# Optimization experiments

Measured on AMD Instinct MI355X. Metric: run time of the kernel, lower is better.

The kernel has to match this reference:

```python
import jax, jax.numpy as jnp
import numpy as np

B, N, Q, M, OUT = 8192, 512, 6, 1024, 256
QUANTILE_COEFFS = np.array([-3.0, -0.834, -0.248, 0.248, 0.834], dtype=np.float32)


def setup_inputs() -> dict:
    key = jax.random.key(0)
    k1, k2, k3, k4, k5, k6, k7 = jax.random.split(key, 7)
    x = jax.random.normal(k1, (B, N), dtype=jnp.float32)
    beta = jnp.zeros((N,), dtype=jnp.float32)
    gamma = jnp.ones((N,), dtype=jnp.float32)
    w = jax.random.normal(k2, (N * Q + M, OUT), dtype=jnp.float32)
    biases = jax.random.normal(k3, (1,), dtype=jnp.float32)
    # chosen_index rows: (count, n1, q1, n2, q2); n-indices in [0,N), q-indices in [0,Q)
    cnt = jnp.arange(M, dtype=jnp.int64)[:, None]
    n1 = jax.random.randint(k4, (M, 1), 0, N)
    q1 = jax.random.randint(k5, (M, 1), 0, Q)
    n2 = jax.random.randint(k6, (M, 1), 0, N)
    q2 = jax.random.randint(k7, (M, 1), 0, Q)
    chosen_index = jnp.concatenate([cnt, n1, q1, n2, q2], axis=1).astype(jnp.int64)
    return {"x": x, "beta": beta, "gamma": gamma, "w": w, "biases": biases,
            "chosen_index": chosen_index}


def reference(x, beta, gamma, w, biases, chosen_index):
    # Batch norm (EMA with decay=0.5 after register+update collapses to batch stats)
    mean = jnp.mean(x, axis=0)                      # (N,)
    var = jnp.var(x, axis=0)                        # (N,) biased, like unbiased=False
    normed = gamma * (x - mean) / jnp.sqrt(var + 0.001) + beta   # (B, N)
    # Maxout: base ReLU + 5 quantile-thresholded branches
    coeffs = jnp.asarray(QUANTILE_COEFFS)           # (5,)
    quant = coeffs[:, None] * var[None, :] + mean[None, :]       # (5, N)
    base = jnp.maximum(0.0, normed)[None]                        # (1, B, N)
    branches = jnp.maximum(0.0, normed[None] - quant[:, None, :] * gamma + beta)  # (5, B, N)
    stacked = jnp.concatenate([base, branches], axis=0)          # (Q, B, N)
    max_x = jnp.transpose(stacked, (1, 2, 0))                    # (B, N, Q)
    # Minout (test mode): per-row gather of two (n,q) coords, elementwise min
    n1, q1 = chosen_index[:, 1], chosen_index[:, 2]
    n2, q2 = chosen_index[:, 3], chosen_index[:, 4]
    D1 = max_x[:, n1, q1]                                        # (B, M)
    D2 = max_x[:, n2, q2]                                        # (B, M)
    min_x = jnp.minimum(D1, D2)                                  # (B, M)
    feat = jnp.concatenate([max_x.reshape(x.shape[0], -1), min_x], axis=1)  # (B, N*Q+M)
    output = feat @ w + biases                                   # (B, OUT)
    return output
```

## Files before the change

kernel.cpp:

```cpp
#include <hip/hip_runtime.h>
#include <stdint.h>

typedef unsigned int uint32;
typedef unsigned short u16;
typedef __attribute__((ext_vector_type(8))) short bf16x8;
typedef __attribute__((ext_vector_type(4))) float f32x4;

#define WS_SCALE 0
#define WS_SHIFT 512
#define WS_SUBQ  1024
#define WS_SHSUB 4096
#define WS_PSUM  8192
#define WS_PSQ   (8192+131072)
#define WRT_OFF  (2u<<20)
#define AMIN_OFF (4u<<20)
#define PART_OFF (21u<<20)

__device__ __forceinline__ u16 f2bf(float f){
  uint32 u; __builtin_memcpy(&u,&f,4);
  u = u + 0x7fffu + ((u>>16)&1u);
  return (u16)(u>>16);
}
__device__ __forceinline__ float bf2f(u16 b){
  uint32 u = ((uint32)b)<<16; float f; __builtin_memcpy(&f,&u,4); return f;
}
__device__ __forceinline__ uint32 pk2(float a, float b){
  return (uint32)f2bf(a) | ((uint32)f2bf(b)<<16);
}
__device__ __forceinline__ void gll16(u16* lds, const u16* g){
  __builtin_amdgcn_global_load_lds((const __attribute__((address_space(1))) uint32*)g,
                                   (__attribute__((address_space(3))) uint32*)lds, 16, 0, 0);
}

__global__ __launch_bounds__(512) void k_pre(const float* __restrict__ x,
                                             const float* __restrict__ w,
                                             float* __restrict__ ws,
                                             u16* __restrict__ wrT){
  int b = blockIdx.x, t = threadIdx.x;
  if (b < 256){
    const float* xp = x + (size_t)b*32*512 + t;
    float sum = 0.f, sq = 0.f;
    #pragma unroll 8
    for (int r=0; r<32; ++r){ float v = xp[(size_t)r*512]; sum += v; sq += v*v; }
    ws[WS_PSUM + b*512 + t] = sum;
    ws[WS_PSQ  + b*512 + t] = sq;
  } else {
    int c2 = b - 256;
    int o = t & 255, half = t >> 8;
    int swzrow = (o >> 1) & 3;
    u16* dst = wrT + (size_t)c2*8192 + o*32;
    #pragma unroll
    for (int gi=0; gi<2; ++gi){
      int g = half*2 + gi;
      union { bf16x8 v; u16 h[8]; } R;
      #pragma unroll
      for (int e=0; e<8; ++e){
        int k = g*8 + e;
        int sk;
        if (c2 < 96) sk = ((c2 & 15)*32 + k)*6 + (c2 >> 4);
        else         sk = 3072 + (c2 - 96)*32 + k;
        R.h[e] = f2bf(w[(size_t)sk*256 + o]);
      }
      *(bf16x8*)(dst + ((g ^ swzrow)*8)) = R.v;
    }
  }
}

__global__ __launch_bounds__(512) void k_stats_final(const float* __restrict__ beta,
                                                     const float* __restrict__ gamma,
                                                     float* __restrict__ ws){
  __shared__ float rs[16][32], rq[16][32];
  int t = threadIdx.x;
  int nl = t & 31, sl = t >> 5;
  int n = blockIdx.x*32 + nl;
  float sum=0.f, sq=0.f;
  #pragma unroll
  for (int j=0;j<16;++j){
    int p = sl*16 + j;
    sum += ws[WS_PSUM + p*512 + n];
    sq  += ws[WS_PSQ  + p*512 + n];
  }
  rs[sl][nl]=sum; rq[sl][nl]=sq;
  __syncthreads();
  if (sl==0){
    #pragma unroll
    for (int j=1;j<16;++j){ sum+=rs[j][nl]; sq+=rq[j][nl]; }
    float mean = sum * (1.0f/8192.0f);
    float var  = sq  * (1.0f/8192.0f) - mean*mean;
    float g = gamma[n], b = beta[n];
    float inv = 1.0f / sqrtf(var + 0.001f);
    float scale = g * inv;
    float shift = b - mean*scale;
    ws[WS_SCALE + n] = scale;
    ws[WS_SHIFT + n] = shift;
    const float QC[5] = {-3.0f, -0.834f, -0.248f, 0.248f, 0.834f};
    ws[WS_SUBQ  + n] = 0.f;
    ws[WS_SHSUB + n] = shift;
    #pragma unroll
    for (int c=0; c<5; ++c){
      float sub = (QC[c]*var + mean)*g - b;
      ws[WS_SUBQ  + (c+1)*512 + n] = sub;
      ws[WS_SHSUB + (c+1)*512 + n] = shift - sub;
    }
  }
}

__global__ __launch_bounds__(256) void k_minfeat(const float* __restrict__ x,
                                                 const float* __restrict__ ws,
                                                 const int* __restrict__ ci,
                                                 u16* __restrict__ amin){
  __shared__ float nrm[8][512];
  __shared__ uint32 tnn[1024];
  __shared__ float ts1[1024];
  __shared__ float ts2[1024];
  int t = threadIdx.x;
  int b0 = blockIdx.x * 8;
  #pragma unroll
  for (int ii=0; ii<4; ++ii){
    int i = ii*256 + t;
    int n1 = ci[i*5+1], q1 = ci[i*5+2], n2 = ci[i*5+3], q2 = ci[i*5+4];
    tnn[i] = (uint32)n1 | ((uint32)n2 << 16);
    ts1[i] = ws[WS_SUBQ + q1*512 + n1];
    ts2[i] = ws[WS_SUBQ + q2*512 + n2];
  }
  {
    int r = t >> 5, c0 = (t & 31) * 16;
    const float* xr = x + (size_t)(b0 + r)*512 + c0;
    #pragma unroll
    for (int j=0;j<4;++j){
      float4 v  = *(const float4*)(xr + j*4);
      float4 sc = *(const float4*)(ws + WS_SCALE + c0 + j*4);
      float4 sh = *(const float4*)(ws + WS_SHIFT + c0 + j*4);
      float4 o; o.x=fmaf(v.x,sc.x,sh.x); o.y=fmaf(v.y,sc.y,sh.y);
      o.z=fmaf(v.z,sc.z,sh.z); o.w=fmaf(v.w,sc.w,sh.w);
      *(float4*)(&nrm[r][c0+j*4]) = o;
    }
  }
  __syncthreads();
  int m0 = t*4;
  uint4  nn = *(const uint4*)(&tnn[m0]);
  float4 s1 = *(const float4*)(&ts1[m0]);
  float4 s2 = *(const float4*)(&ts2[m0]);
  int cc = m0 >> 5, k = m0 & 31, g2 = k >> 3;
  #pragma unroll
  for (int r=0;r<8;++r){
    float v0 = fminf(fmaxf(nrm[r][nn.x & 0xffff] - s1.x, 0.f), fmaxf(nrm[r][nn.x >> 16] - s2.x, 0.f));
    float v1 = fminf(fmaxf(nrm[r][nn.y & 0xffff] - s1.y, 0.f), fmaxf(nrm[r][nn.y >> 16] - s2.y, 0.f));
    float v2 = fminf(fmaxf(nrm[r][nn.z & 0xffff] - s1.z, 0.f), fmaxf(nrm[r][nn.z >> 16] - s2.z, 0.f));
    float v3 = fminf(fmaxf(nrm[r][nn.w & 0xffff] - s1.w, 0.f), fmaxf(nrm[r][nn.w >> 16] - s2.w, 0.f));
    int pos = cc*32 + ((g2 ^ (((b0 + r) >> 1) & 3))*8) + (k & 7);
    uint2 pv; pv.x = pk2(v0,v1); pv.y = pk2(v2,v3);
    *(uint2*)(amin + (size_t)(b0 + r)*1024 + pos) = pv;
  }
}

__global__ __launch_bounds__(512,4) void k_gemm(const float* __restrict__ x,
                                                const float* __restrict__ ws,
                                                const u16* __restrict__ wrT,
                                                const u16* __restrict__ amin,
                                                u16* __restrict__ parts){
  __shared__ u16 wt[2][8192];
  __shared__ u16 ft[2][4096];
  __shared__ float pscale[512];
  __shared__ float pshsub[512];

  int t = threadIdx.x;
  int d = blockIdx.x;
  int mtile = d & 63, s = d >> 6;
  int brow = mtile * 128;
  bool isMin = (s >= 6);

  if (!isMin){
    pscale[t] = ws[WS_SCALE + t];
    pshsub[t] = ws[WS_SHSUB + s*512 + t];
  }

  int row = t >> 2, g = t & 3;
  int ftw = row*32 + ((g ^ ((row >> 1) & 3))*8);
  int wuni = t & ~63;
  const float* xrow = x + (size_t)(brow + row)*512;
  const u16* aminrow = amin + (size_t)(brow + row)*1024 + (isMin ? (s-6)*512 : 0) + g*8;
  const u16* wbase = wrT + (size_t)(s*16)*8192;

  int lane = t & 63, wv = t >> 6;
  int wm = wv >> 2, wn = wv & 3;
  int lr = lane & 15, lk = lane >> 4;
  int g16 = (lk ^ ((lr >> 1) & 3)) * 8;
  f32x4 acc[4][4] = {};
  float4 xa[2][2];

  auto loadX = [&](int cc, int xb){
    int col = cc*32 + g*8;
    xa[xb][0] = *(const float4*)(xrow + col);
    xa[xb][1] = *(const float4*)(xrow + col + 4);
  };
  auto stageW = [&](int cc, int nb){
    const u16* wsrc = wbase + (size_t)cc*8192;
    gll16(&wt[nb][wuni*8], wsrc + (size_t)t*8);
    gll16(&wt[nb][4096 + wuni*8], wsrc + 4096 + (size_t)t*8);
    if (isMin) gll16(&ft[nb][wuni*8], aminrow + cc*32);
  };
  auto packFT = [&](int cc, int nb, int xb){
    int col = cc*32 + g*8;
    float4 a0 = xa[xb][0], a1 = xa[xb][1];
    float4 sc0 = *(const float4*)(pscale + col);
    float4 sc1 = *(const float4*)(pscale + col + 4);
    float4 h0  = *(const float4*)(pshsub + col);
    float4 h1  = *(const float4*)(pshsub + col + 4);
    union { bf16x8 v; uint32 u[4]; } R;
    R.u[0] = pk2(fmaxf(fmaf(a0.x,sc0.x,h0.x),0.f), fmaxf(fmaf(a0.y,sc0.y,h0.y),0.f));
    R.u[1] = pk2(fmaxf(fmaf(a0.z,sc0.z,h0.z),0.f), fmaxf(fmaf(a0.w,sc0.w,h0.w),0.f));
    R.u[2] = pk2(fmaxf(fmaf(a1.x,sc1.x,h1.x),0.f), fmaxf(fmaf(a1.y,sc1.y,h1.y),0.f));
    R.u[3] = pk2(fmaxf(fmaf(a1.z,sc1.z,h1.z),0.f), fmaxf(fmaf(a1.w,sc1.w,h1.w),0.f));
    *(bf16x8*)(&ft[nb][ftw]) = R.v;
  };
  auto compute = [&](int cb){
    bf16x8 A[4], Bv[4];
    #pragma unroll
    for (int mi=0; mi<4; ++mi)
      A[mi] = *(const bf16x8*)(&ft[cb][(wm*64 + mi*16 + lr)*32 + g16]);
    #pragma unroll
    for (int ni=0; ni<4; ++ni)
      Bv[ni] = *(const bf16x8*)(&wt[cb][(wn*64 + ni*16 + lr)*32 + g16]);
    #pragma unroll
    for (int mi=0; mi<4; ++mi)
      #pragma unroll
      for (int ni=0; ni<4; ++ni)
        acc[mi][ni] = __builtin_amdgcn_mfma_f32_16x16x32_bf16(A[mi], Bv[ni], acc[mi][ni], 0, 0, 0);
  };

  __syncthreads();
  if (!isMin) loadX(0, 0);
  stageW(0, 0);
  if (!isMin){ packFT(0, 0, 0); loadX(1, 1); }
  __syncthreads();

  int cur = 0;
  for (int c=0; c<16; ++c){
    if (!isMin && c < 14) loadX(c+2, c & 1);
    if (c < 15){
      stageW(c+1, cur^1);
      if (!isMin) packFT(c+1, cur^1, (c+1) & 1);
    }
    compute(cur);
    __syncthreads();
    cur ^= 1;
  }

  u16* pp = parts + ((size_t)s*8192 + brow)*256;
  #pragma unroll
  for (int mi=0; mi<4; ++mi)
    #pragma unroll
    for (int ni=0; ni<4; ++ni)
      #pragma unroll
      for (int r=0; r<4; ++r){
        int rl = wm*64 + mi*16 + lk*4 + r;
        int cl = wn*64 + ni*16 + lr;
        pp[(size_t)rl*256 + cl] = f2bf(acc[mi][ni][r]);
      }
}

__global__ __launch_bounds__(256) void k_reduce(const u16* __restrict__ parts,
                                                const float* __restrict__ biases,
                                                float* __restrict__ out){
  int i = (blockIdx.x*256 + threadIdx.x) * 8;
  float b = biases[0];
  float a[8];
  #pragma unroll
  for (int j=0;j<8;++j) a[j] = b;
  #pragma unroll
  for (int s2=0;s2<8;++s2){
    bf16x8 v = *(const bf16x8*)(parts + (size_t)s2*2097152 + i);
    #pragma unroll
    for (int j=0;j<8;++j) a[j] += bf2f((u16)v[j]);
  }
  float4 o0 = {a[0],a[1],a[2],a[3]}, o1 = {a[4],a[5],a[6],a[7]};
  *(float4*)(out + i) = o0;
  *(float4*)(out + i + 4) = o1;
}

extern "C" void kernel_launch(void* const* d_in, const int* in_sizes, int n_in,
                              void* d_out, int out_size, void* d_ws, size_t ws_size,
                              hipStream_t stream){
  const float* x      = (const float*)d_in[0];
  const float* beta   = (const float*)d_in[1];
  const float* gamma  = (const float*)d_in[2];
  const float* w      = (const float*)d_in[3];
  const float* biases = (const float*)d_in[4];
  const int*   ci     = (const int*)d_in[5];
  float* out = (float*)d_out;
  float* wsf = (float*)d_ws;
  u16* wrT   = (u16*)((char*)d_ws + WRT_OFF);
  u16* amin  = (u16*)((char*)d_ws + AMIN_OFF);
  u16* parts = (u16*)((char*)d_ws + PART_OFF);

  k_pre         <<<384, 512, 0, stream>>>(x, w, wsf, wrT);
  k_stats_final <<<16,  512, 0, stream>>>(beta, gamma, wsf);
  k_minfeat     <<<1024,256, 0, stream>>>(x, wsf, ci, amin);
  k_gemm        <<<512, 512, 0, stream>>>(x, wsf, wrT, amin, parts);
  k_reduce      <<<1024,256, 0, stream>>>(parts, biases, out);
}
```

Measured before the change: 54.55 us.

## Fuse split-K reduction into GEMM via last-block atomic counter

```diff
diff --git a/kernel.cpp b/kernel.cpp
--- a/kernel.cpp
+++ b/kernel.cpp
@@ -12,6 +12,7 @@
 #define WS_SHSUB 4096
 #define WS_PSUM  8192
 #define WS_PSQ   (8192+131072)
+#define CNT_OFF  0x180000u
 #define WRT_OFF  (2u<<20)
 #define AMIN_OFF (4u<<20)
 #define PART_OFF (21u<<20)
@@ -158,11 +159,15 @@
                                                 const float* __restrict__ ws,
                                                 const u16* __restrict__ wrT,
                                                 const u16* __restrict__ amin,
-                                                u16* __restrict__ parts){
+                                                const float* __restrict__ biases,
+                                                u16* __restrict__ parts,
+                                                int* __restrict__ cnt,
+                                                float* __restrict__ out){
   __shared__ u16 wt[2][8192];
   __shared__ u16 ft[2][4096];
   __shared__ float pscale[512];
   __shared__ float pshsub[512];
+  __shared__ int lastFlag;
 
   int t = threadIdx.x;
   int d = blockIdx.x;
@@ -258,25 +263,37 @@
         int cl = wn*64 + ni*16 + lr;
         pp[(size_t)rl*256 + cl] = f2bf(acc[mi][ni][r]);
       }
-}
-
-__global__ __launch_bounds__(256) void k_reduce(const u16* __restrict__ parts,
-                                                const float* __restrict__ biases,
-                                                float* __restrict__ out){
-  int i = (blockIdx.x*256 + threadIdx.x) * 8;
-  float b = biases[0];
-  float a[8];
-  #pragma unroll
-  for (int j=0;j<8;++j) a[j] = b;
-  #pragma unroll
-  for (int s2=0;s2<8;++s2){
-    bf16x8 v = *(const bf16x8*)(parts + (size_t)s2*2097152 + i);
-    #pragma unroll
-    for (int j=0;j<8;++j) a[j] += bf2f((u16)v[j]);
-  }
-  float4 o0 = {a[0],a[1],a[2],a[3]}, o1 = {a[4],a[5],a[6],a[7]};
-  *(float4*)(out + i) = o0;
-  *(float4*)(out + i + 4) = o1;
+
+  __threadfence();
+  __syncthreads();
+  if (t == 0){
+    int old = atomicAdd(cnt + mtile, 1);
+    lastFlag = (old == 7);
+  }
+  __syncthreads();
+  if (lastFlag){
+    __threadfence();
+    float b0 = biases[0];
+    const u16* pb = parts + (size_t)brow*256;
+    float* op = out + (size_t)brow*256;
+    #pragma unroll
+    for (int it=0; it<8; ++it){
+      int task = it*512 + t;
+      int rowi = task >> 5, cg = task & 31;
+      float a[8];
+      #pragma unroll
+      for (int j=0;j<8;++j) a[j] = b0;
+      #pragma unroll
+      for (int s2=0;s2<8;++s2){
+        bf16x8 v = *(const bf16x8*)(pb + (size_t)s2*2097152 + rowi*256 + cg*8);
+        #pragma unroll
+        for (int j=0;j<8;++j) a[j] += bf2f((u16)v[j]);
+      }
+      float4 o0 = {a[0],a[1],a[2],a[3]}, o1 = {a[4],a[5],a[6],a[7]};
+      *(float4*)(op + rowi*256 + cg*8) = o0;
+      *(float4*)(op + rowi*256 + cg*8 + 4) = o1;
+    }
+  }
 }
 
 extern "C" void kernel_launch(void* const* d_in, const int* in_sizes, int n_in,
@@ -293,10 +310,11 @@
   u16* wrT   = (u16*)((char*)d_ws + WRT_OFF);
   u16* amin  = (u16*)((char*)d_ws + AMIN_OFF);
   u16* parts = (u16*)((char*)d_ws + PART_OFF);
-
+  int* cnt   = (int*)((char*)d_ws + CNT_OFF);
+
+  hipMemsetAsync(cnt, 0, 64*sizeof(int), stream);
   k_pre         <<<384, 512, 0, stream>>>(x, w, wsf, wrT);
   k_stats_final <<<16,  512, 0, stream>>>(beta, gamma, wsf);
   k_minfeat     <<<1024,256, 0, stream>>>(x, wsf, ci, amin);
-  k_gemm        <<<512, 512, 0, stream>>>(x, wsf, wrT, amin, parts);
-  k_reduce      <<<1024,256, 0, stream>>>(parts, biases, out);
-}
+  k_gemm        <<<512, 512, 0, stream>>>(x, wsf, wrT, amin, biases, parts, cnt, out);
+}
```

New measurement: 214.3 us. 3.93x slower.

## Fuse min-feature computation into GEMM blocks that consume it

Applied to the files above, without the earlier changes.

```diff
diff --git a/kernel.cpp b/kernel.cpp
--- a/kernel.cpp
+++ b/kernel.cpp
@@ -105,59 +105,11 @@
   }
 }
 
-__global__ __launch_bounds__(256) void k_minfeat(const float* __restrict__ x,
-                                                 const float* __restrict__ ws,
-                                                 const int* __restrict__ ci,
-                                                 u16* __restrict__ amin){
-  __shared__ float nrm[8][512];
-  __shared__ uint32 tnn[1024];
-  __shared__ float ts1[1024];
-  __shared__ float ts2[1024];
-  int t = threadIdx.x;
-  int b0 = blockIdx.x * 8;
-  #pragma unroll
-  for (int ii=0; ii<4; ++ii){
-    int i = ii*256 + t;
-    int n1 = ci[i*5+1], q1 = ci[i*5+2], n2 = ci[i*5+3], q2 = ci[i*5+4];
-    tnn[i] = (uint32)n1 | ((uint32)n2 << 16);
-    ts1[i] = ws[WS_SUBQ + q1*512 + n1];
-    ts2[i] = ws[WS_SUBQ + q2*512 + n2];
-  }
-  {
-    int r = t >> 5, c0 = (t & 31) * 16;
-    const float* xr = x + (size_t)(b0 + r)*512 + c0;
-    #pragma unroll
-    for (int j=0;j<4;++j){
-      float4 v  = *(const float4*)(xr + j*4);
-      float4 sc = *(const float4*)(ws + WS_SCALE + c0 + j*4);
-      float4 sh = *(const float4*)(ws + WS_SHIFT + c0 + j*4);
-      float4 o; o.x=fmaf(v.x,sc.x,sh.x); o.y=fmaf(v.y,sc.y,sh.y);
-      o.z=fmaf(v.z,sc.z,sh.z); o.w=fmaf(v.w,sc.w,sh.w);
-      *(float4*)(&nrm[r][c0+j*4]) = o;
-    }
-  }
-  __syncthreads();
-  int m0 = t*4;
-  uint4  nn = *(const uint4*)(&tnn[m0]);
-  float4 s1 = *(const float4*)(&ts1[m0]);
-  float4 s2 = *(const float4*)(&ts2[m0]);
-  int cc = m0 >> 5, k = m0 & 31, g2 = k >> 3;
-  #pragma unroll
-  for (int r=0;r<8;++r){
-    float v0 = fminf(fmaxf(nrm[r][nn.x & 0xffff] - s1.x, 0.f), fmaxf(nrm[r][nn.x >> 16] - s2.x, 0.f));
-    float v1 = fminf(fmaxf(nrm[r][nn.y & 0xffff] - s1.y, 0.f), fmaxf(nrm[r][nn.y >> 16] - s2.y, 0.f));
-    float v2 = fminf(fmaxf(nrm[r][nn.z & 0xffff] - s1.z, 0.f), fmaxf(nrm[r][nn.z >> 16] - s2.z, 0.f));
-    float v3 = fminf(fmaxf(nrm[r][nn.w & 0xffff] - s1.w, 0.f), fmaxf(nrm[r][nn.w >> 16] - s2.w, 0.f));
-    int pos = cc*32 + ((g2 ^ (((b0 + r) >> 1) & 3))*8) + (k & 7);
-    uint2 pv; pv.x = pk2(v0,v1); pv.y = pk2(v2,v3);
-    *(uint2*)(amin + (size_t)(b0 + r)*1024 + pos) = pv;
-  }
-}
-
 __global__ __launch_bounds__(512,4) void k_gemm(const float* __restrict__ x,
                                                 const float* __restrict__ ws,
                                                 const u16* __restrict__ wrT,
-                                                const u16* __restrict__ amin,
+                                                const int* __restrict__ ci,
+                                                u16* __restrict__ amin,
                                                 u16* __restrict__ parts){
   __shared__ u16 wt[2][8192];
   __shared__ u16 ft[2][4096];
@@ -173,6 +125,59 @@
   if (!isMin){
     pscale[t] = ws[WS_SCALE + t];
     pshsub[t] = ws[WS_SHSUB + s*512 + t];
+  } else {
+    int h = s - 6;
+    float*  nrmL = (float*)&wt[0][0];
+    uint32* tnnL = (uint32*)&ft[0][0];
+    float*  ts1L = (float*)&ft[0][0] + 512;
+    float*  ts2L = (float*)&ft[0][0] + 1024;
+    {
+      int gm = h*512 + t;
+      int n1 = ci[gm*5+1], q1 = ci[gm*5+2], n2 = ci[gm*5+3], q2 = ci[gm*5+4];
+      tnnL[t] = (uint32)n1 | ((uint32)n2 << 16);
+      ts1L[t] = ws[WS_SUBQ + q1*512 + n1];
+      ts2L[t] = ws[WS_SUBQ + q2*512 + n2];
+    }
+    int pr = t >> 6;
+    int c0 = (t & 63) * 8;
+    float4 sc0 = *(const float4*)(ws + WS_SCALE + c0);
+    float4 sc1 = *(const float4*)(ws + WS_SCALE + c0 + 4);
+    float4 sh0 = *(const float4*)(ws + WS_SHIFT + c0);
+    float4 sh1 = *(const float4*)(ws + WS_SHIFT + c0 + 4);
+    __syncthreads();
+    uint32 nn[8]; float g1[8], g2v[8];
+    #pragma unroll
+    for (int j=0;j<8;++j){ nn[j]=tnnL[c0+j]; g1[j]=ts1L[c0+j]; g2v[j]=ts2L[c0+j]; }
+    int gm0 = h*512 + c0;
+    int posb = (gm0 >> 5)*32 + (c0 & 31);
+    int g2s = (c0 & 31) >> 3;
+    for (int p=0; p<16; ++p){
+      int grow = brow + p*8 + pr;
+      const float* xr = x + (size_t)grow*512 + c0;
+      float4 v0 = *(const float4*)xr;
+      float4 v1 = *(const float4*)(xr + 4);
+      float4 o0, o1;
+      o0.x=fmaf(v0.x,sc0.x,sh0.x); o0.y=fmaf(v0.y,sc0.y,sh0.y);
+      o0.z=fmaf(v0.z,sc0.z,sh0.z); o0.w=fmaf(v0.w,sc0.w,sh0.w);
+      o1.x=fmaf(v1.x,sc1.x,sh1.x); o1.y=fmaf(v1.y,sc1.y,sh1.y);
+      o1.z=fmaf(v1.z,sc1.z,sh1.z); o1.w=fmaf(v1.w,sc1.w,sh1.w);
+      *(float4*)(&nrmL[pr*512 + c0]) = o0;
+      *(float4*)(&nrmL[pr*512 + c0 + 4]) = o1;
+      __syncthreads();
+      const float* nr = &nrmL[pr*512];
+      union { bf16x8 v; uint32 u[4]; } R;
+      #pragma unroll
+      for (int j=0;j<8;j+=2){
+        float a0 = fminf(fmaxf(nr[nn[j] & 0xffff]   - g1[j],   0.f),
+                         fmaxf(nr[nn[j] >> 16]      - g2v[j],  0.f));
+        float a1 = fminf(fmaxf(nr[nn[j+1] & 0xffff] - g1[j+1], 0.f),
+                         fmaxf(nr[nn[j+1] >> 16]    - g2v[j+1],0.f));
+        R.u[j>>1] = pk2(a0, a1);
+      }
+      int pos = (gm0 >> 5)*32 + ((g2s ^ ((grow >> 1) & 3))*8);
+      *(bf16x8*)(amin + (size_t)grow*1024 + pos) = R.v;
+      __syncthreads();
+    }
   }
 
   int row = t >> 2, g = t & 3;
@@ -296,7 +301,6 @@
 
   k_pre         <<<384, 512, 0, stream>>>(x, w, wsf, wrT);
   k_stats_final <<<16,  512, 0, stream>>>(beta, gamma, wsf);
-  k_minfeat     <<<1024,256, 0, stream>>>(x, wsf, ci, amin);
-  k_gemm        <<<512, 512, 0, stream>>>(x, wsf, wrT, amin, parts);
+  k_gemm        <<<512, 512, 0, stream>>>(x, wsf, wrT, ci, amin, parts);
   k_reduce      <<<1024,256, 0, stream>>>(parts, biases, out);
 }
```

New measurement: 58.19 us. 6.7% more time.
